# Kernel optimization log

Measured on AMD Instinct MI355X. Metric: run time of the kernel, lower is better.

Reference implementation:

```python
import jax, jax.numpy as jnp
import numpy as np

B, K, N, D, H, NNEG, NTOP = 8, 8, 128, 256, 128, 64, 64
UNARY_SCALES = (1.0, 1.0, 1.0)  # one scale per tree level, tree_height = log2(K) = 3


def setup_inputs():
    key = jax.random.key(0)
    ks = jax.random.split(key, 8)
    s = 0.05
    return {
        'pos_fea': jax.random.normal(ks[0], (B, K, N, D), jnp.float32),
        'neg_fea': jax.random.normal(ks[1], (B * K, NNEG, D), jnp.float32),
        'pos_classes': jax.random.randint(ks[2], (B, K, N), 0, 20),
        'target_class': jax.random.randint(ks[3], (B,), 0, 20),
        'Wp1': jax.random.normal(ks[4], (2 * D, H), jnp.float32) * s,
        'bp1': jnp.zeros((H,), jnp.float32),
        'Wp2': jax.random.normal(ks[5], (H, 1), jnp.float32) * s,
        'bp2': jnp.zeros((1,), jnp.float32),
        'Wu1': jax.random.normal(ks[6], (2 * D, H), jnp.float32) * s,
        'bu1': jnp.zeros((H,), jnp.float32),
        'Wu2': jax.random.normal(ks[7], (H, 1), jnp.float32) * s,
        'bu2': jnp.zeros((1,), jnp.float32),
    }


def _relation(f0, f1, W1, b1, W2, b2):
    # RelationModule: Dense(H, relu) -> Dense(1) applied to concat([f0_m, f1_n])
    # for every cross pair; concat-Dense is split into two GEMMs. -> [Bn, M0, M1]
    d = f0.shape[-1]
    h0 = jnp.einsum('bmd,dh->bmh', f0, W1[:d])
    h1 = jnp.einsum('bnd,dh->bnh', f1, W1[d:])
    h = jax.nn.relu(h0[:, :, None, :] + h1[:, None, :, :] + b1)
    return jnp.einsum('bmnh,h->bmn', h, W2[:, 0]) + b2[0]


def _bg(t, idx):
    # batched_gather along axis 1: t [Bn, P, ...], idx [Bn, T]
    ie = idx.reshape(idx.shape + (1,) * (t.ndim - 2))
    ie = jnp.broadcast_to(ie, idx.shape + t.shape[2:])
    return jnp.take_along_axis(t, ie, axis=1)


def _rep(fea, sub):
    # subproblem representative feature: fea [Bn,S,N,D], sub [Bn,M,S] -> [Bn,M,D]
    idx = jnp.swapaxes(sub, 1, 2)[..., None]              # [Bn,S,M,1]
    idx = jnp.broadcast_to(idx, idx.shape[:-1] + (fea.shape[-1],))
    return jnp.take_along_axis(fea, idx, axis=2).mean(axis=1)


def _tree(pos_fea, neg_fea, Wp1, bp1, Wp2, bp2, Wu1, bu1, Wu2, bu2):
    pos_flat = pos_fea.reshape(B * K, N, D)
    # UnaryModule: mean relation score of each positive proposal vs the negative bag
    ue = _relation(pos_flat, neg_fea, Wu1, bu1, Wu2, bu2).mean(-1)   # [B*K, N]
    sub = jnp.broadcast_to(jnp.arange(N, dtype=jnp.int32)[None, :, None], (B * K, N, 1))
    pe = jnp.zeros_like(ue)
    tree_height = int(np.log2(K))
    best = None
    for i in range(tree_height):
        S = 2 ** i                      # subproblem size per branch at this level
        Bn = sub.shape[0] // 2
        M = sub.shape[1]
        sub2 = sub.reshape(Bn, 2, M, S)  # [::2] / [1::2] split of adjacent rows
        sub0, sub1 = sub2[:, 0], sub2[:, 1]
        pe2 = pe.reshape(Bn, 2, M)
        ue2 = ue.reshape(Bn, 2, M)
        fea = pos_flat.reshape(Bn, 2, S, N, D)
        rep0 = _rep(fea[:, 0], sub0)
        rep1 = _rep(fea[:, 1], sub1)
        # PairwiseCrossSimilarity: scores for all cross pairs of candidates
        scores = _relation(rep0, rep1, Wp1, bp1, Wp2, bp2).reshape(Bn, M * M)
        p0 = jnp.repeat(jnp.arange(M), M)
        p1 = jnp.tile(jnp.arange(M), M)
        pe = pe2[:, 0][:, p0] + pe2[:, 1][:, p1] - scores
        ue = ue2[:, 0][:, p0] + ue2[:, 1][:, p1]
        total = pe + UNARY_SCALES[i] * ue
        sub = jnp.concatenate([sub0[:, p0], sub1[:, p1]], axis=-1)  # [Bn, M*M, 2S]
        topk = 1 if i == tree_height - 1 else min(M * M, NTOP)
        _, inds = jax.lax.top_k(-total, topk)
        sub = _bg(sub, inds)
        ue = jnp.take_along_axis(ue, inds, axis=1)
        pe = jnp.take_along_axis(pe, inds, axis=1)
        best = jnp.take_along_axis(total, inds, axis=1)
    return sub, best


def reference(pos_fea, neg_fea, pos_classes, target_class,
              Wp1, bp1, Wp2, bp2, Wu1, bu1, Wu2, bu2):
    sub, _ = _tree(pos_fea, neg_fea, Wp1, bp1, Wp2, bp2, Wu1, bu1, Wu2, bu2)
    is_target = (pos_classes == target_class[:, None, None]).astype(jnp.float32)
    return sub[:, 0], is_target  # selected proposal per image [B,K], [B,K,N]
```

## Files before the change

### kernel.cpp

```cpp
#include <hip/hip_runtime.h>
#include <stdint.h>

#define B_ 8
#define K_ 8
#define N_ 128
#define D_ 256
#define H_ 128
#define NNEG_ 64

typedef unsigned long long u64;

__device__ __forceinline__ u64 shfl_xor_u64(u64 v, int m) {
    int lo = __shfl_xor((int)(unsigned)v, m, 64);
    int hi = __shfl_xor((int)(unsigned)(v >> 32), m, 64);
    return ((u64)(unsigned)hi << 32) | (unsigned)lo;
}
__device__ __forceinline__ u64 bitonic_merge64(u64 m, int lane) {
#pragma unroll
    for (int j = 32; j > 0; j >>= 1) {
        u64 o = shfl_xor_u64(m, j);
        bool keepMin = ((lane & j) == 0);
        bool lt = m < o;
        m = (keepMin == lt) ? m : o;
    }
    return m;
}
__device__ __forceinline__ unsigned sortable(float f) {
    unsigned u = __float_as_uint(f);
    return (u & 0x80000000u) ? ~u : (u | 0x80000000u);
}
__device__ __forceinline__ float unsortable(unsigned u) {
    return __uint_as_float((u & 0x80000000u) ? (u & 0x7FFFFFFFu) : ~u);
}
__device__ __forceinline__ void sort128_wave0(u64* cand, int cc, int lane) {
    u64 v0 = (lane < cc) ? cand[lane] : ~0ull;
    u64 v1 = (64 + lane < cc) ? cand[64 + lane] : ~0ull;
#pragma unroll
    for (int k = 2; k <= 64; k <<= 1) {
        bool d0 = ((lane & k) == 0);
        bool d1 = (k == 64) ? false : d0;
#pragma unroll
        for (int j = k >> 1; j > 0; j >>= 1) {
            u64 o0 = shfl_xor_u64(v0, j);
            bool km0 = (((lane & j) == 0) == d0);
            v0 = (km0 == (v0 < o0)) ? v0 : o0;
            u64 o1 = shfl_xor_u64(v1, j);
            bool km1 = (((lane & j) == 0) == d1);
            v1 = (km1 == (v1 < o1)) ? v1 : o1;
        }
    }
    if (v0 > v1) { u64 tmp = v0; v0 = v1; v1 = tmp; }
#pragma unroll
    for (int j = 32; j > 0; j >>= 1) {
        bool km = ((lane & j) == 0);
        u64 o0 = shfl_xor_u64(v0, j);
        v0 = (km == (v0 < o0)) ? v0 : o0;
        u64 o1 = shfl_xor_u64(v1, j);
        v1 = (km == (v1 < o1)) ? v1 : o1;
    }
    cand[lane] = v0; cand[64 + lane] = v1;
}

__global__ __launch_bounds__(256) void g1_gemm(
    const float* __restrict__ pos, const float* __restrict__ neg,
    const float* __restrict__ Wu1, const float* __restrict__ Wp1,
    const int* __restrict__ pos_classes, const int* __restrict__ target_class,
    float* __restrict__ HU0, float* __restrict__ HU1n,
    float* __restrict__ HP0, float* __restrict__ HP1,
    float* __restrict__ outp) {
    int bid = blockIdx.x;
    int t = threadIdx.x;
    if (bid >= 448) {
        int base = (bid - 448) * 2048 + t * 8;
#pragma unroll
        for (int q = 0; q < 8; ++q) {
            int idx = base + q;
            outp[64 + idx] = (pos_classes[idx] == target_class[idx >> 10]) ? 1.0f : 0.0f;
        }
        return;
    }
    const float* A; const float* W; float* OUT; int rb;
    if (bid < 128)      { A = pos; W = Wu1;           OUT = HU0;  rb = bid * 64; }
    else if (bid < 192) { A = neg; W = Wu1 + D_ * H_; OUT = HU1n; rb = (bid - 128) * 64; }
    else if (bid < 320) { A = pos; W = Wp1;           OUT = HP0;  rb = (bid - 192) * 64; }
    else                { A = pos; W = Wp1 + D_ * H_; OUT = HP1;  rb = (bid - 320) * 64; }

    __shared__ float As[64][17];
    __shared__ float Bs[16][128];
    int tx = t & 15, ty = t >> 4;
    float acc[4][8];
#pragma unroll
    for (int i = 0; i < 4; ++i)
#pragma unroll
        for (int j = 0; j < 8; ++j) acc[i][j] = 0.f;

    for (int k0 = 0; k0 < D_; k0 += 16) {
        {
            int row = t >> 2, kq = (t & 3) * 4;
            const float4 av = *(const float4*)&A[(size_t)(rb + row) * D_ + k0 + kq];
            As[row][kq + 0] = av.x; As[row][kq + 1] = av.y;
            As[row][kq + 2] = av.z; As[row][kq + 3] = av.w;
        }
        {
            int flat = t * 8;
            int kr = flat >> 7, hc = flat & 127;
            float4 b0 = *(const float4*)&W[(size_t)(k0 + kr) * H_ + hc];
            float4 b1 = *(const float4*)&W[(size_t)(k0 + kr) * H_ + hc + 4];
            *(float4*)&Bs[kr][hc] = b0;
            *(float4*)&Bs[kr][hc + 4] = b1;
        }
        __syncthreads();
#pragma unroll
        for (int kk = 0; kk < 16; ++kk) {
            float a0 = As[ty * 4 + 0][kk], a1 = As[ty * 4 + 1][kk];
            float a2 = As[ty * 4 + 2][kk], a3 = As[ty * 4 + 3][kk];
            float bv[8];
            *(float4*)&bv[0] = *(const float4*)&Bs[kk][tx * 8];
            *(float4*)&bv[4] = *(const float4*)&Bs[kk][tx * 8 + 4];
#pragma unroll
            for (int j = 0; j < 8; ++j) {
                acc[0][j] += a0 * bv[j];
                acc[1][j] += a1 * bv[j];
                acc[2][j] += a2 * bv[j];
                acc[3][j] += a3 * bv[j];
            }
        }
        __syncthreads();
    }
#pragma unroll
    for (int i = 0; i < 4; ++i) {
        float4 o0 = {acc[i][0], acc[i][1], acc[i][2], acc[i][3]};
        float4 o1 = {acc[i][4], acc[i][5], acc[i][6], acc[i][7]};
        *(float4*)&OUT[(size_t)(rb + ty * 4 + i) * H_ + tx * 8] = o0;
        *(float4*)&OUT[(size_t)(rb + ty * 4 + i) * H_ + tx * 8 + 4] = o1;
    }
}

__global__ __launch_bounds__(256) void g2_ue_sc0(
    const float* __restrict__ HU0, const float* __restrict__ HU1n,
    const float* __restrict__ bu1, const float* __restrict__ Wu2,
    const float* __restrict__ bu2v,
    const float* __restrict__ HP0, const float* __restrict__ HP1,
    const float* __restrict__ bp1, const float* __restrict__ Wp2,
    const float* __restrict__ bp2,
    float* __restrict__ t0, float* __restrict__ sc0) {
    __shared__ float smem[13568];
    float (*Ls)[129] = (float(*)[129])smem;
    float (*Rs)[129] = (float(*)[129])(smem + 4128);
    float* wsv = smem + 4128 + 8256;
    float (*red)[33] = (float(*)[33])(smem + 4128 + 8256 + 128);

    int bid = blockIdx.x;
    int t = threadIdx.x;
    bool is_ue = bid < 256;

    if (is_ue) {
        int bk = bid >> 2, mt = bid & 3;
        for (int i = t; i < 64 * 128; i += 256) {
            int n = i >> 7, h = i & 127;
            Rs[n][h] = HU1n[(size_t)(bk * NNEG_ + n) * H_ + h];
        }
        for (int i = t; i < 32 * 128; i += 256) {
            int m = i >> 7, h = i & 127;
            Ls[m][h] = HU0[(size_t)(bk * N_ + mt * 32 + m) * H_ + h] + bu1[h];
        }
        if (t < 128) wsv[t] = Wu2[t];
    } else {
        int bid2 = bid - 256;
        int b = bid2 >> 3, m0t = (bid2 >> 1) & 3, m1t = bid2 & 1;
        const float* Lg = HP0 + (size_t)b * 2 * N_ * H_ + m0t * 32 * H_;
        const float* Rg = HP1 + (size_t)b * 2 * N_ * H_ + N_ * H_ + m1t * 64 * H_;
        for (int i = t; i < 64 * 128; i += 256) {
            int n = i >> 7, h = i & 127;
            Rs[n][h] = Rg[(size_t)n * H_ + h];
        }
        for (int i = t; i < 32 * 128; i += 256) {
            int m = i >> 7, h = i & 127;
            Ls[m][h] = Lg[(size_t)m * H_ + h] + bp1[h];
        }
        if (t < 128) wsv[t] = Wp2[t];
    }
    __syncthreads();

    int tm = t & 7, tn = t >> 3;
    const float* l0 = &Ls[tm * 4 + 0][0];
    const float* l1 = &Ls[tm * 4 + 1][0];
    const float* l2 = &Ls[tm * 4 + 2][0];
    const float* l3 = &Ls[tm * 4 + 3][0];
    const float* r0 = &Rs[tn * 2 + 0][0];
    const float* r1 = &Rs[tn * 2 + 1][0];
    float a00 = 0.f, a01 = 0.f, a10 = 0.f, a11 = 0.f;
    float a20 = 0.f, a21 = 0.f, a30 = 0.f, a31 = 0.f;
#pragma unroll 4
    for (int h = 0; h < 128; ++h) {
        float w = wsv[h];
        float b0 = r0[h], b1 = r1[h];
        float a0 = l0[h], a1 = l1[h], a2 = l2[h], a3 = l3[h];
        float v;
        v = a0 + b0; v = v > 0.f ? v : 0.f; a00 += v * w;
        v = a0 + b1; v = v > 0.f ? v : 0.f; a01 += v * w;
        v = a1 + b0; v = v > 0.f ? v : 0.f; a10 += v * w;
        v = a1 + b1; v = v > 0.f ? v : 0.f; a11 += v * w;
        v = a2 + b0; v = v > 0.f ? v : 0.f; a20 += v * w;
        v = a2 + b1; v = v > 0.f ? v : 0.f; a21 += v * w;
        v = a3 + b0; v = v > 0.f ? v : 0.f; a30 += v * w;
        v = a3 + b1; v = v > 0.f ? v : 0.f; a31 += v * w;
    }

    if (is_ue) {
        int bk = bid >> 2, mt = bid & 3;
        red[tm * 4 + 0][tn] = a00 + a01;
        red[tm * 4 + 1][tn] = a10 + a11;
        red[tm * 4 + 2][tn] = a20 + a21;
        red[tm * 4 + 3][tn] = a30 + a31;
        __syncthreads();
        if (t < 32) {
            float s = 0.f;
            for (int q = 0; q < 32; ++q) s += red[t][q];
            t0[bk * N_ + mt * 32 + t] = s * (1.0f / NNEG_) + bu2v[0];
        }
    } else {
        int bid2 = bid - 256;
        int b = bid2 >> 3, m0t = (bid2 >> 1) & 3, m1t = bid2 & 1;
        float bp2v = bp2[0];
        float* orow = sc0 + (size_t)b * 16384;
        float accs[4][2] = {{a00, a01}, {a10, a11}, {a20, a21}, {a30, a31}};
#pragma unroll
        for (int i = 0; i < 4; ++i) {
            int m0 = m0t * 32 + tm * 4 + i;
#pragma unroll
            for (int j = 0; j < 2; ++j) {
                int m1 = m1t * 64 + tn * 2 + j;
                orow[m0 * 128 + m1] = accs[i][j] + bp2v;
            }
        }
    }
}

__global__ __launch_bounds__(1024) void g3_top0(const float* __restrict__ sc0,
                                                const float* __restrict__ t0,
                                                float* __restrict__ tA,
                                                int* __restrict__ pA) {
    int r = blockIdx.x;
    int t = threadIdx.x, lane = t & 63;
    __shared__ float tt[256];
    __shared__ unsigned cnt[16][2];
    __shared__ unsigned ccnt;
    __shared__ u64 cand[128];
    if (t < 256) tt[t] = t0[r * 256 + t];
    if (t < 32) cnt[t >> 1][t & 1] = 0u;
    if (t == 0) ccnt = 0u;
    __syncthreads();
    const float* row = sc0 + (size_t)r * 16384;
    unsigned sv[16];
#pragma unroll
    for (int j = 0; j < 16; ++j) {
        int idx = j * 1024 + t;
        float v = (tt[idx >> 7] + tt[128 + (idx & 127)]) - row[idx];
        sv[j] = sortable(v);
    }
    unsigned T = 0u;
#pragma unroll
    for (int it = 0; it < 16; ++it) {
        int p = 30 - 2 * it;
        unsigned C1 = T | (1u << p), C2 = T | (2u << p), C3 = T | (3u << p);
        unsigned c13 = 0u, c2 = 0u;
#pragma unroll
        for (int j = 0; j < 16; ++j) {
            c13 += (sv[j] < C1) ? 1u : 0u;
            c13 += (sv[j] < C3) ? 0x10000u : 0u;
            c2 += (sv[j] < C2) ? 1u : 0u;
        }
#pragma unroll
        for (int off = 32; off > 0; off >>= 1) {
            c13 += (unsigned)__shfl_xor((int)c13, off, 64);
            c2 += (unsigned)__shfl_xor((int)c2, off, 64);
        }
        if (lane == 0) { atomicAdd(&cnt[it][0], c13); atomicAdd(&cnt[it][1], c2); }
        __syncthreads();
        unsigned t13 = cnt[it][0], t2v = cnt[it][1];
        unsigned t1 = t13 & 0xFFFFu, t3 = t13 >> 16;
        unsigned k = (t3 < 64u) ? 3u : (t2v < 64u) ? 2u : (t1 < 64u) ? 1u : 0u;
        T |= (k << p);
    }
#pragma unroll
    for (int j = 0; j < 16; ++j) {
        if (sv[j] <= T) {
            unsigned pos = atomicAdd(&ccnt, 1u);
            if (pos < 128u) {
                int idx = j * 1024 + t;
                cand[pos] = ((u64)sv[j] << 32) | (unsigned)idx;
            }
        }
    }
    __syncthreads();
    if (t < 64) {
        int cc = (int)(ccnt < 128u ? ccnt : 128u);
        sort128_wave0(cand, cc, lane);
        u64 kk = cand[lane];
        int idx = (int)(kk & 0xFFFFFFFFull);
        tA[r * 64 + lane] = unsortable((unsigned)(kk >> 32));
        pA[r * 64 + lane] = ((idx >> 7) << 8) | (idx & 127);
    }
}

__global__ __launch_bounds__(256) void g4a_s1(
    const float* __restrict__ HP0, const float* __restrict__ HP1,
    const float* __restrict__ tA, const int* __restrict__ pA,
    const float* __restrict__ bp1, const float* __restrict__ Wp2,
    const float* __restrict__ bp2, u64* __restrict__ g4top) {
    int bid = blockIdx.x;
    int u = bid >> 1, half = bid & 1;
    int t = threadIdx.x, lane = t & 63, w = t >> 6;
    __shared__ float LsT[128][68];
    __shared__ float RsT[128][36];
    __shared__ float taL[64], taR[64];
    __shared__ int paL[64], paR[64];
    __shared__ float wsv[128];
    __shared__ unsigned cnt[16][2];
    __shared__ unsigned ccnt;
    __shared__ u64 cand[128];
    if (t < 64) { taL[t] = tA[(2 * u) * 64 + t]; paL[t] = pA[(2 * u) * 64 + t]; }
    else if (t < 128) { int e = t - 64; taR[e] = tA[(2 * u + 1) * 64 + e]; paR[e] = pA[(2 * u + 1) * 64 + e]; }
    if (t < 128) wsv[t] = Wp2[t];
    if (t < 32) cnt[t >> 1][t & 1] = 0u;
    if (t == 0) ccnt = 0u;
    float bp2v = bp2[0];
    __syncthreads();
    for (int i = t; i < 64 * 128; i += 256) {
        int m = i >> 7, h = i & 127;
        int pk = paL[m]; int a0 = pk >> 8, a1 = pk & 255;
        float s = HP0[(size_t)(4 * u) * 16384 + a0 * 128 + h]
                + HP0[(size_t)(4 * u + 1) * 16384 + a1 * 128 + h];
        LsT[h][m] = s * 0.5f + bp1[h];
    }
    for (int i = t; i < 32 * 128; i += 256) {
        int n = i >> 7, h = i & 127;
        int ng = half * 32 + n;
        int pk = paR[ng]; int c0 = pk >> 8, c1 = pk & 255;
        float s = HP1[(size_t)(4 * u + 2) * 16384 + c0 * 128 + h]
                + HP1[(size_t)(4 * u + 3) * 16384 + c1 * 128 + h];
        RsT[h][n] = s * 0.5f;
    }
    __syncthreads();
    int qm = w * 4 + (lane >> 4);
    int qn = lane & 15;
    float acc[4][2];
#pragma unroll
    for (int i = 0; i < 4; ++i) { acc[i][0] = 0.f; acc[i][1] = 0.f; }
#pragma unroll 2
    for (int h = 0; h < 128; ++h) {
        float4 lv = *(const float4*)&LsT[h][qm * 4];
        float2 rv = *(const float2*)&RsT[h][qn * 2];
        float wv = wsv[h];
        float v;
        v = lv.x + rv.x; v = v > 0.f ? v : 0.f; acc[0][0] += v * wv;
        v = lv.x + rv.y; v = v > 0.f ? v : 0.f; acc[0][1] += v * wv;
        v = lv.y + rv.x; v = v > 0.f ? v : 0.f; acc[1][0] += v * wv;
        v = lv.y + rv.y; v = v > 0.f ? v : 0.f; acc[1][1] += v * wv;
        v = lv.z + rv.x; v = v > 0.f ? v : 0.f; acc[2][0] += v * wv;
        v = lv.z + rv.y; v = v > 0.f ? v : 0.f; acc[2][1] += v * wv;
        v = lv.w + rv.x; v = v > 0.f ? v : 0.f; acc[3][0] += v * wv;
        v = lv.w + rv.y; v = v > 0.f ? v : 0.f; acc[3][1] += v * wv;
    }
    unsigned sv[8];
#pragma unroll
    for (int mi = 0; mi < 4; ++mi) {
#pragma unroll
        for (int nj = 0; nj < 2; ++nj) {
            int m = qm * 4 + mi;
            int ng = half * 32 + qn * 2 + nj;
            float val = (taL[m] + taR[ng]) - (acc[mi][nj] + bp2v);
            sv[mi * 2 + nj] = sortable(val);
        }
    }
    unsigned T = 0u;
#pragma unroll
    for (int it = 0; it < 16; ++it) {
        int p = 30 - 2 * it;
        unsigned C1 = T | (1u << p), C2 = T | (2u << p), C3 = T | (3u << p);
        unsigned c13 = 0u, c2 = 0u;
#pragma unroll
        for (int j = 0; j < 8; ++j) {
            c13 += (sv[j] < C1) ? 1u : 0u;
            c13 += (sv[j] < C3) ? 0x10000u : 0u;
            c2 += (sv[j] < C2) ? 1u : 0u;
        }
#pragma unroll
        for (int off = 32; off > 0; off >>= 1) {
            c13 += (unsigned)__shfl_xor((int)c13, off, 64);
            c2 += (unsigned)__shfl_xor((int)c2, off, 64);
        }
        if (lane == 0) { atomicAdd(&cnt[it][0], c13); atomicAdd(&cnt[it][1], c2); }
        __syncthreads();
        unsigned t13 = cnt[it][0], t2v = cnt[it][1];
        unsigned t1 = t13 & 0xFFFFu, t3 = t13 >> 16;
        unsigned k = (t3 < 64u) ? 3u : (t2v < 64u) ? 2u : (t1 < 64u) ? 1u : 0u;
        T |= (k << p);
    }
#pragma unroll
    for (int j = 0; j < 8; ++j) {
        if (sv[j] <= T) {
            unsigned pos = atomicAdd(&ccnt, 1u);
            if (pos < 128u) {
                int mi = j >> 1, nj = j & 1;
                int idx = (qm * 4 + mi) * 64 + half * 32 + qn * 2 + nj;
                cand[pos] = ((u64)sv[j] << 32) | (unsigned)idx;
            }
        }
    }
    __syncthreads();
    if (w == 0) {
        int cc = (int)(ccnt < 128u ? ccnt : 128u);
        sort128_wave0(cand, cc, lane);
        g4top[(size_t)bid * 64 + lane] = cand[lane];
    }
}

__global__ __launch_bounds__(256) void g4b_s2(
    const float* __restrict__ HP0, const float* __restrict__ HP1,
    const int* __restrict__ pA, const u64* __restrict__ g4top,
    const float* __restrict__ bp1, const float* __restrict__ Wp2,
    const float* __restrict__ bp2, float* __restrict__ outp) {
    int b = blockIdx.x;
    int t = threadIdx.x, lane = t & 63, w = t >> 6;
    __shared__ float LsT[128][68];
    __shared__ float RsT[128][36];
    __shared__ float tL[64], tR[64];
    __shared__ unsigned subL[64], subR[64];
    __shared__ float wsv[128];
    __shared__ u64 sred[4];
    if (t < 128) wsv[t] = Wp2[t];
    float bp2v = bp2[0];
    if (w < 2) {
        const u64* A = g4top + (size_t)(4 * b + 2 * w) * 64;
        const u64* Bp = g4top + (size_t)(4 * b + 2 * w + 1) * 64;
        u64 x = A[lane], y = Bp[63 - lane];
        u64 m = x < y ? x : y;
        m = bitonic_merge64(m, lane);
        int idx = (int)(m & 0xFFFFFFFFull);
        int p0 = idx >> 6, p1 = idx & 63;
        float val = unsortable((unsigned)(m >> 32));
        int rowL = 4 * b + 2 * w;
        int pkL = pA[rowL * 64 + p0];
        int pkR = pA[(rowL + 1) * 64 + p1];
        unsigned leaves = ((unsigned)pkL << 16) | (unsigned)pkR;
        if (w == 0) { tL[lane] = val; subL[lane] = leaves; }
        else        { tR[lane] = val; subR[lane] = leaves; }
    }
    __syncthreads();
    for (int i = t; i < 64 * 128; i += 256) {
        int m = i >> 7, h = i & 127;
        unsigned s4 = subL[m];
        float s = HP0[(size_t)(8 * b + 0) * 16384 + ((s4 >> 24) & 255u) * 128 + h]
                + HP0[(size_t)(8 * b + 1) * 16384 + ((s4 >> 16) & 255u) * 128 + h]
                + HP0[(size_t)(8 * b + 2) * 16384 + ((s4 >> 8) & 255u) * 128 + h]
                + HP0[(size_t)(8 * b + 3) * 16384 + (s4 & 255u) * 128 + h];
        LsT[h][m] = s * 0.25f + bp1[h];
    }
    u64 best = ~0ull;
    int qm = w * 4 + (lane >> 4);
    int qn = lane & 15;
    for (int half = 0; half < 2; ++half) {
        __syncthreads();
        for (int i = t; i < 32 * 128; i += 256) {
            int n = i >> 7, h = i & 127;
            int ng = half * 32 + n;
            unsigned s4 = subR[ng];
            float s = HP1[(size_t)(8 * b + 4) * 16384 + ((s4 >> 24) & 255u) * 128 + h]
                    + HP1[(size_t)(8 * b + 5) * 16384 + ((s4 >> 16) & 255u) * 128 + h]
                    + HP1[(size_t)(8 * b + 6) * 16384 + ((s4 >> 8) & 255u) * 128 + h]
                    + HP1[(size_t)(8 * b + 7) * 16384 + (s4 & 255u) * 128 + h];
            RsT[h][n] = s * 0.25f;
        }
        __syncthreads();
        float acc[4][2];
#pragma unroll
        for (int i = 0; i < 4; ++i) { acc[i][0] = 0.f; acc[i][1] = 0.f; }
#pragma unroll 2
        for (int h = 0; h < 128; ++h) {
            float4 lv = *(const float4*)&LsT[h][qm * 4];
            float2 rv = *(const float2*)&RsT[h][qn * 2];
            float wv = wsv[h];
            float v;
            v = lv.x + rv.x; v = v > 0.f ? v : 0.f; acc[0][0] += v * wv;
            v = lv.x + rv.y; v = v > 0.f ? v : 0.f; acc[0][1] += v * wv;
            v = lv.y + rv.x; v = v > 0.f ? v : 0.f; acc[1][0] += v * wv;
            v = lv.y + rv.y; v = v > 0.f ? v : 0.f; acc[1][1] += v * wv;
            v = lv.z + rv.x; v = v > 0.f ? v : 0.f; acc[2][0] += v * wv;
            v = lv.z + rv.y; v = v > 0.f ? v : 0.f; acc[2][1] += v * wv;
            v = lv.w + rv.x; v = v > 0.f ? v : 0.f; acc[3][0] += v * wv;
            v = lv.w + rv.y; v = v > 0.f ? v : 0.f; acc[3][1] += v * wv;
        }
#pragma unroll
        for (int mi = 0; mi < 4; ++mi) {
#pragma unroll
            for (int nj = 0; nj < 2; ++nj) {
                int m = qm * 4 + mi;
                int ng = half * 32 + qn * 2 + nj;
                float val = (tL[m] + tR[ng]) - (acc[mi][nj] + bp2v);
                u64 kk = ((u64)sortable(val) << 32) | (unsigned)(m * 64 + ng);
                best = kk < best ? kk : best;
            }
        }
    }
#pragma unroll
    for (int off = 32; off > 0; off >>= 1) {
        u64 o = shfl_xor_u64(best, off);
        best = o < best ? o : best;
    }
    if (lane == 0) sred[w] = best;
    __syncthreads();
    if (t == 0) {
        u64 bb = sred[0];
        for (int p = 1; p < 4; ++p) { u64 o = sred[p]; bb = o < bb ? o : bb; }
        int idx = (int)(bb & 0xFFFFFFFFull);
        unsigned sl = subL[idx >> 6], sr = subR[idx & 63];
        outp[b * 8 + 0] = (float)((sl >> 24) & 255u);
        outp[b * 8 + 1] = (float)((sl >> 16) & 255u);
        outp[b * 8 + 2] = (float)((sl >> 8) & 255u);
        outp[b * 8 + 3] = (float)(sl & 255u);
        outp[b * 8 + 4] = (float)((sr >> 24) & 255u);
        outp[b * 8 + 5] = (float)((sr >> 16) & 255u);
        outp[b * 8 + 6] = (float)((sr >> 8) & 255u);
        outp[b * 8 + 7] = (float)(sr & 255u);
    }
}

extern "C" void kernel_launch(void* const* d_in, const int* in_sizes, int n_in,
                              void* d_out, int out_size, void* d_ws, size_t ws_size,
                              hipStream_t stream) {
    const float* pos = (const float*)d_in[0];
    const float* neg = (const float*)d_in[1];
    const int* pos_classes = (const int*)d_in[2];
    const int* target_class = (const int*)d_in[3];
    const float* Wp1 = (const float*)d_in[4];
    const float* bp1 = (const float*)d_in[5];
    const float* Wp2 = (const float*)d_in[6];
    const float* bp2 = (const float*)d_in[7];
    const float* Wu1 = (const float*)d_in[8];
    const float* bu1 = (const float*)d_in[9];
    const float* Wu2 = (const float*)d_in[10];
    const float* bu2 = (const float*)d_in[11];

    float* wsf = (float*)d_ws;
    float* HU0 = wsf;
    float* HP0 = HU0 + 1048576;
    float* HP1 = HP0 + 1048576;
    float* HU1n = HP1 + 1048576;
    float* t0 = HU1n + 524288;
    float* sc0 = t0 + 8192;
    float* tA = sc0 + 524288;
    int* pA = (int*)(tA + 2048);
    u64* g4top = (u64*)(pA + 2048);
    float* outp = (float*)d_out;

    g1_gemm<<<452, 256, 0, stream>>>(pos, neg, Wu1, Wp1, pos_classes,
                                     target_class, HU0, HU1n, HP0, HP1, outp);
    g2_ue_sc0<<<512, 256, 0, stream>>>(HU0, HU1n, bu1, Wu2, bu2,
                                       HP0, HP1, bp1, Wp2, bp2, t0, sc0);
    g3_top0<<<32, 1024, 0, stream>>>(sc0, t0, tA, pA);
    g4a_s1<<<32, 256, 0, stream>>>(HP0, HP1, tA, pA, bp1, Wp2, bp2, g4top);
    g4b_s2<<<8, 256, 0, stream>>>(HP0, HP1, pA, g4top, bp1, Wp2, bp2, outp);
}
```

Before: 209.2 us.

## Split top-k selection across more blocks with per-wave select and merge trees

The level-0 top-64 selection now runs per wave on 512-element chunks across 256 blocks. Each wave does a ballot-based radix select with no block barriers, then bitonic-sorts its candidates, and a separate small kernel merges the 8 partial lists per row. The level-1 pair scoring is spread over 128 blocks with smaller tiles, and its radix select is replaced by a direct 128-element register sort per wave plus merges. The intent is to lift the low block counts and the barrier- and atomic-heavy selection loops. In exchange it adds one more launch and an extra global round trip for the partial lists, and it reuses the start of the workspace (HU0) for the candidate buffers.

```diff
diff --git a/kernel.cpp b/kernel.cpp
--- a/kernel.cpp
+++ b/kernel.cpp
@@ -25,6 +25,11 @@
     }
     return m;
 }
+__device__ __forceinline__ u64 merge2(u64 a, u64 b, int lane) {
+    u64 br = shfl_xor_u64(b, 63);
+    u64 m = a < br ? a : br;
+    return bitonic_merge64(m, lane);
+}
 __device__ __forceinline__ unsigned sortable(float f) {
     unsigned u = __float_as_uint(f);
     return (u & 0x80000000u) ? ~u : (u | 0x80000000u);
@@ -32,9 +37,7 @@
 __device__ __forceinline__ float unsortable(unsigned u) {
     return __uint_as_float((u & 0x80000000u) ? (u & 0x7FFFFFFFu) : ~u);
 }
-__device__ __forceinline__ void sort128_wave0(u64* cand, int cc, int lane) {
-    u64 v0 = (lane < cc) ? cand[lane] : ~0ull;
-    u64 v1 = (64 + lane < cc) ? cand[64 + lane] : ~0ull;
+__device__ __forceinline__ void sort128_reg(u64& v0, u64& v1, int lane) {
 #pragma unroll
     for (int k = 2; k <= 64; k <<= 1) {
         bool d0 = ((lane & k) == 0);
@@ -58,7 +61,6 @@
         u64 o1 = shfl_xor_u64(v1, j);
         v1 = (km == (v1 < o1)) ? v1 : o1;
     }
-    cand[lane] = v0; cand[64 + lane] = v1;
 }
 
 __global__ __launch_bounds__(256) void g1_gemm(
@@ -237,71 +239,83 @@
     }
 }
 
-__global__ __launch_bounds__(1024) void g3_top0(const float* __restrict__ sc0,
+__global__ __launch_bounds__(256) void g3a_top0(const float* __restrict__ sc0,
                                                 const float* __restrict__ t0,
+                                                u64* __restrict__ g3c) {
+    int bid = blockIdx.x;
+    int r = bid >> 3, c = bid & 7;
+    int t = threadIdx.x, lane = t & 63, w = t >> 6;
+    __shared__ float tt[256];
+    __shared__ u64 cand[4][128];
+    if (t < 256) tt[t] = t0[r * 256 + t];
+    __syncthreads();
+    const float* row = sc0 + (size_t)r * 16384 + c * 2048 + w * 512;
+    unsigned sv[8];
+#pragma unroll
+    for (int j = 0; j < 8; ++j) {
+        int li = j * 64 + lane;
+        int idx = c * 2048 + w * 512 + li;
+        float v = (tt[idx >> 7] + tt[128 + (idx & 127)]) - row[li];
+        sv[j] = sortable(v);
+    }
+    unsigned T = 0u;
+#pragma unroll
+    for (int it = 0; it < 16; ++it) {
+        int p = 30 - 2 * it;
+        unsigned C1 = T | (1u << p), C2 = T | (2u << p), C3 = T | (3u << p);
+        unsigned c1 = 0u, c2 = 0u, c3 = 0u;
+#pragma unroll
+        for (int j = 0; j < 8; ++j) {
+            c1 += (unsigned)__popcll(__ballot(sv[j] < C1));
+            c2 += (unsigned)__popcll(__ballot(sv[j] < C2));
+            c3 += (unsigned)__popcll(__ballot(sv[j] < C3));
+        }
+        unsigned k = (c3 < 64u) ? 3u : (c2 < 64u) ? 2u : (c1 < 64u) ? 1u : 0u;
+        T |= (k << p);
+    }
+    u64* my = cand[w];
+    int base = 0;
+#pragma unroll
+    for (int j = 0; j < 8; ++j) {
+        u64 mask = __ballot(sv[j] <= T);
+        if (sv[j] <= T) {
+            int pos = base + (int)__popcll(mask & ((1ull << lane) - 1ull));
+            if (pos < 128) {
+                int idx = c * 2048 + w * 512 + j * 64 + lane;
+                my[pos] = ((u64)sv[j] << 32) | (unsigned)idx;
+            }
+        }
+        base += (int)__popcll(mask);
+    }
+    int cc = base < 128 ? base : 128;
+    u64 v0 = (lane < cc) ? my[lane] : ~0ull;
+    u64 v1 = (64 + lane < cc) ? my[64 + lane] : ~0ull;
+    sort128_reg(v0, v1, lane);
+    my[lane] = v0;
+    __syncthreads();
+    if (w == 0) {
+        u64 x0 = cand[0][lane], x1 = cand[1][lane];
+        u64 x2 = cand[2][lane], x3 = cand[3][lane];
+        u64 y0 = merge2(x0, x1, lane), y1 = merge2(x2, x3, lane);
+        g3c[(size_t)bid * 64 + lane] = merge2(y0, y1, lane);
+    }
+}
+
+__global__ __launch_bounds__(64) void g3b_merge(const u64* __restrict__ g3c,
                                                 float* __restrict__ tA,
                                                 int* __restrict__ pA) {
     int r = blockIdx.x;
-    int t = threadIdx.x, lane = t & 63;
-    __shared__ float tt[256];
-    __shared__ unsigned cnt[16][2];
-    __shared__ unsigned ccnt;
-    __shared__ u64 cand[128];
-    if (t < 256) tt[t] = t0[r * 256 + t];
-    if (t < 32) cnt[t >> 1][t & 1] = 0u;
-    if (t == 0) ccnt = 0u;
-    __syncthreads();
-    const float* row = sc0 + (size_t)r * 16384;
-    unsigned sv[16];
-#pragma unroll
-    for (int j = 0; j < 16; ++j) {
-        int idx = j * 1024 + t;
-        float v = (tt[idx >> 7] + tt[128 + (idx & 127)]) - row[idx];
-        sv[j] = sortable(v);
-    }
-    unsigned T = 0u;
-#pragma unroll
-    for (int it = 0; it < 16; ++it) {
-        int p = 30 - 2 * it;
-        unsigned C1 = T | (1u << p), C2 = T | (2u << p), C3 = T | (3u << p);
-        unsigned c13 = 0u, c2 = 0u;
-#pragma unroll
-        for (int j = 0; j < 16; ++j) {
-            c13 += (sv[j] < C1) ? 1u : 0u;
-            c13 += (sv[j] < C3) ? 0x10000u : 0u;
-            c2 += (sv[j] < C2) ? 1u : 0u;
-        }
-#pragma unroll
-        for (int off = 32; off > 0; off >>= 1) {
-            c13 += (unsigned)__shfl_xor((int)c13, off, 64);
-            c2 += (unsigned)__shfl_xor((int)c2, off, 64);
-        }
-        if (lane == 0) { atomicAdd(&cnt[it][0], c13); atomicAdd(&cnt[it][1], c2); }
-        __syncthreads();
-        unsigned t13 = cnt[it][0], t2v = cnt[it][1];
-        unsigned t1 = t13 & 0xFFFFu, t3 = t13 >> 16;
-        unsigned k = (t3 < 64u) ? 3u : (t2v < 64u) ? 2u : (t1 < 64u) ? 1u : 0u;
-        T |= (k << p);
-    }
-#pragma unroll
-    for (int j = 0; j < 16; ++j) {
-        if (sv[j] <= T) {
-            unsigned pos = atomicAdd(&ccnt, 1u);
-            if (pos < 128u) {
-                int idx = j * 1024 + t;
-                cand[pos] = ((u64)sv[j] << 32) | (unsigned)idx;
-            }
-        }
-    }
-    __syncthreads();
-    if (t < 64) {
-        int cc = (int)(ccnt < 128u ? ccnt : 128u);
-        sort128_wave0(cand, cc, lane);
-        u64 kk = cand[lane];
-        int idx = (int)(kk & 0xFFFFFFFFull);
-        tA[r * 64 + lane] = unsortable((unsigned)(kk >> 32));
-        pA[r * 64 + lane] = ((idx >> 7) << 8) | (idx & 127);
-    }
+    int lane = threadIdx.x;
+    const u64* Lp = g3c + (size_t)r * 512;
+    u64 x0 = Lp[lane], x1 = Lp[64 + lane], x2 = Lp[128 + lane], x3 = Lp[192 + lane];
+    u64 x4 = Lp[256 + lane], x5 = Lp[320 + lane], x6 = Lp[384 + lane], x7 = Lp[448 + lane];
+    u64 y0 = merge2(x0, x1, lane), y1 = merge2(x2, x3, lane);
+    u64 y2 = merge2(x4, x5, lane), y3 = merge2(x6, x7, lane);
+    u64 z0 = merge2(y0, y1, lane), z1 = merge2(y2, y3, lane);
+    u64 f = merge2(z0, z1, lane);
+    int idx = (int)(f & 0xFFFFFFFFull);
+    tA[r * 64 + lane] = unsortable((unsigned)(f >> 32));
+    pA[r * 64 + lane] = ((idx >> 7) << 8) | (idx & 127);
 }
 
 __global__ __launch_bounds__(256) void g4a_s1(
@@ -310,24 +324,20 @@
     const float* __restrict__ bp1, const float* __restrict__ Wp2,
     const float* __restrict__ bp2, u64* __restrict__ g4top) {
     int bid = blockIdx.x;
-    int u = bid >> 1, half = bid & 1;
+    int u = bid >> 3, mq = (bid >> 1) & 3, nh = bid & 1;
     int t = threadIdx.x, lane = t & 63, w = t >> 6;
-    __shared__ float LsT[128][68];
-    __shared__ float RsT[128][36];
-    __shared__ float taL[64], taR[64];
-    __shared__ int paL[64], paR[64];
+    __shared__ float LsT[128][17];
+    __shared__ float RsT[128][34];
+    __shared__ float taL[16], taR[32];
+    __shared__ int paL[16], paR[32];
     __shared__ float wsv[128];
-    __shared__ unsigned cnt[16][2];
-    __shared__ unsigned ccnt;
-    __shared__ u64 cand[128];
-    if (t < 64) { taL[t] = tA[(2 * u) * 64 + t]; paL[t] = pA[(2 * u) * 64 + t]; }
-    else if (t < 128) { int e = t - 64; taR[e] = tA[(2 * u + 1) * 64 + e]; paR[e] = pA[(2 * u + 1) * 64 + e]; }
-    if (t < 128) wsv[t] = Wp2[t];
-    if (t < 32) cnt[t >> 1][t & 1] = 0u;
-    if (t == 0) ccnt = 0u;
+    __shared__ u64 cand[4][64];
+    if (t < 16) { taL[t] = tA[(2 * u) * 64 + mq * 16 + t]; paL[t] = pA[(2 * u) * 64 + mq * 16 + t]; }
+    else if (t < 48) { int e = t - 16; taR[e] = tA[(2 * u + 1) * 64 + nh * 32 + e]; paR[e] = pA[(2 * u + 1) * 64 + nh * 32 + e]; }
+    if (t >= 128) wsv[t - 128] = Wp2[t - 128];
     float bp2v = bp2[0];
     __syncthreads();
-    for (int i = t; i < 64 * 128; i += 256) {
+    for (int i = t; i < 16 * 128; i += 256) {
         int m = i >> 7, h = i & 127;
         int pk = paL[m]; int a0 = pk >> 8, a1 = pk & 255;
         float s = HP0[(size_t)(4 * u) * 16384 + a0 * 128 + h]
@@ -336,84 +346,38 @@
     }
     for (int i = t; i < 32 * 128; i += 256) {
         int n = i >> 7, h = i & 127;
-        int ng = half * 32 + n;
-        int pk = paR[ng]; int c0 = pk >> 8, c1 = pk & 255;
+        int pk = paR[n]; int c0 = pk >> 8, c1 = pk & 255;
         float s = HP1[(size_t)(4 * u + 2) * 16384 + c0 * 128 + h]
                 + HP1[(size_t)(4 * u + 3) * 16384 + c1 * 128 + h];
         RsT[h][n] = s * 0.5f;
     }
     __syncthreads();
-    int qm = w * 4 + (lane >> 4);
-    int qn = lane & 15;
-    float acc[4][2];
-#pragma unroll
-    for (int i = 0; i < 4; ++i) { acc[i][0] = 0.f; acc[i][1] = 0.f; }
-#pragma unroll 2
+    int lm = w * 4 + (lane >> 4);
+    int ln = lane & 15;
+    float a0 = 0.f, a1 = 0.f;
+#pragma unroll 4
     for (int h = 0; h < 128; ++h) {
-        float4 lv = *(const float4*)&LsT[h][qm * 4];
-        float2 rv = *(const float2*)&RsT[h][qn * 2];
+        float lv = LsT[h][lm];
+        float2 rv = *(const float2*)&RsT[h][ln * 2];
         float wv = wsv[h];
         float v;
-        v = lv.x + rv.x; v = v > 0.f ? v : 0.f; acc[0][0] += v * wv;
-        v = lv.x + rv.y; v = v > 0.f ? v : 0.f; acc[0][1] += v * wv;
-        v = lv.y + rv.x; v = v > 0.f ? v : 0.f; acc[1][0] += v * wv;
-        v = lv.y + rv.y; v = v > 0.f ? v : 0.f; acc[1][1] += v * wv;
-        v = lv.z + rv.x; v = v > 0.f ? v : 0.f; acc[2][0] += v * wv;
-        v = lv.z + rv.y; v = v > 0.f ? v : 0.f; acc[2][1] += v * wv;
-        v = lv.w + rv.x; v = v > 0.f ? v : 0.f; acc[3][0] += v * wv;
-        v = lv.w + rv.y; v = v > 0.f ? v : 0.f; acc[3][1] += v * wv;
-    }
-    unsigned sv[8];
-#pragma unroll
-    for (int mi = 0; mi < 4; ++mi) {
-#pragma unroll
-        for (int nj = 0; nj < 2; ++nj) {
-            int m = qm * 4 + mi;
-            int ng = half * 32 + qn * 2 + nj;
-            float val = (taL[m] + taR[ng]) - (acc[mi][nj] + bp2v);
-            sv[mi * 2 + nj] = sortable(val);
-        }
-    }
-    unsigned T = 0u;
-#pragma unroll
-    for (int it = 0; it < 16; ++it) {
-        int p = 30 - 2 * it;
-        unsigned C1 = T | (1u << p), C2 = T | (2u << p), C3 = T | (3u << p);
-        unsigned c13 = 0u, c2 = 0u;
-#pragma unroll
-        for (int j = 0; j < 8; ++j) {
-            c13 += (sv[j] < C1) ? 1u : 0u;
-            c13 += (sv[j] < C3) ? 0x10000u : 0u;
-            c2 += (sv[j] < C2) ? 1u : 0u;
-        }
-#pragma unroll
-        for (int off = 32; off > 0; off >>= 1) {
-            c13 += (unsigned)__shfl_xor((int)c13, off, 64);
-            c2 += (unsigned)__shfl_xor((int)c2, off, 64);
-        }
-        if (lane == 0) { atomicAdd(&cnt[it][0], c13); atomicAdd(&cnt[it][1], c2); }
-        __syncthreads();
-        unsigned t13 = cnt[it][0], t2v = cnt[it][1];
-        unsigned t1 = t13 & 0xFFFFu, t3 = t13 >> 16;
-        unsigned k = (t3 < 64u) ? 3u : (t2v < 64u) ? 2u : (t1 < 64u) ? 1u : 0u;
-        T |= (k << p);
-    }
-#pragma unroll
-    for (int j = 0; j < 8; ++j) {
-        if (sv[j] <= T) {
-            unsigned pos = atomicAdd(&ccnt, 1u);
-            if (pos < 128u) {
-                int mi = j >> 1, nj = j & 1;
-                int idx = (qm * 4 + mi) * 64 + half * 32 + qn * 2 + nj;
-                cand[pos] = ((u64)sv[j] << 32) | (unsigned)idx;
-            }
-        }
-    }
+        v = lv + rv.x; v = v > 0.f ? v : 0.f; a0 += v * wv;
+        v = lv + rv.y; v = v > 0.f ? v : 0.f; a1 += v * wv;
+    }
+    int m_unit = mq * 16 + lm;
+    int n0 = nh * 32 + ln * 2;
+    float val0 = (taL[lm] + taR[ln * 2 + 0]) - (a0 + bp2v);
+    float val1 = (taL[lm] + taR[ln * 2 + 1]) - (a1 + bp2v);
+    u64 v0 = ((u64)sortable(val0) << 32) | (unsigned)(m_unit * 64 + n0);
+    u64 v1 = ((u64)sortable(val1) << 32) | (unsigned)(m_unit * 64 + n0 + 1);
+    sort128_reg(v0, v1, lane);
+    cand[w][lane] = v0;
     __syncthreads();
     if (w == 0) {
-        int cc = (int)(ccnt < 128u ? ccnt : 128u);
-        sort128_wave0(cand, cc, lane);
-        g4top[(size_t)bid * 64 + lane] = cand[lane];
+        u64 x0 = cand[0][lane], x1 = cand[1][lane];
+        u64 x2 = cand[2][lane], x3 = cand[3][lane];
+        u64 y0 = merge2(x0, x1, lane), y1 = merge2(x2, x3, lane);
+        g4top[(size_t)bid * 64 + lane] = merge2(y0, y1, lane);
     }
 }
 
@@ -433,11 +397,13 @@
     if (t < 128) wsv[t] = Wp2[t];
     float bp2v = bp2[0];
     if (w < 2) {
-        const u64* A = g4top + (size_t)(4 * b + 2 * w) * 64;
-        const u64* Bp = g4top + (size_t)(4 * b + 2 * w + 1) * 64;
-        u64 x = A[lane], y = Bp[63 - lane];
-        u64 m = x < y ? x : y;
-        m = bitonic_merge64(m, lane);
+        const u64* Lp = g4top + (size_t)(2 * b + w) * 512;
+        u64 x0 = Lp[lane], x1 = Lp[64 + lane], x2 = Lp[128 + lane], x3 = Lp[192 + lane];
+        u64 x4 = Lp[256 + lane], x5 = Lp[320 + lane], x6 = Lp[384 + lane], x7 = Lp[448 + lane];
+        u64 y0 = merge2(x0, x1, lane), y1 = merge2(x2, x3, lane);
+        u64 y2 = merge2(x4, x5, lane), y3 = merge2(x6, x7, lane);
+        u64 z0 = merge2(y0, y1, lane), z1 = merge2(y2, y3, lane);
+        u64 m = merge2(z0, z1, lane);
         int idx = (int)(m & 0xFFFFFFFFull);
         int p0 = idx >> 6, p1 = idx & 63;
         float val = unsortable((unsigned)(m >> 32));
@@ -552,14 +518,16 @@
     float* sc0 = t0 + 8192;
     float* tA = sc0 + 524288;
     int* pA = (int*)(tA + 2048);
-    u64* g4top = (u64*)(pA + 2048);
+    u64* g3c = (u64*)wsf;
+    u64* g4top = (u64*)wsf + 16384;
     float* outp = (float*)d_out;
 
     g1_gemm<<<452, 256, 0, stream>>>(pos, neg, Wu1, Wp1, pos_classes,
                                      target_class, HU0, HU1n, HP0, HP1, outp);
     g2_ue_sc0<<<512, 256, 0, stream>>>(HU0, HU1n, bu1, Wu2, bu2,
                                        HP0, HP1, bp1, Wp2, bp2, t0, sc0);
-    g3_top0<<<32, 1024, 0, stream>>>(sc0, t0, tA, pA);
-    g4a_s1<<<32, 256, 0, stream>>>(HP0, HP1, tA, pA, bp1, Wp2, bp2, g4top);
+    g3a_top0<<<256, 256, 0, stream>>>(sc0, t0, g3c);
+    g3b_merge<<<32, 64, 0, stream>>>(g3c, tA, pA);
+    g4a_s1<<<128, 256, 0, stream>>>(HP0, HP1, tA, pA, bp1, Wp2, bp2, g4top);
     g4b_s2<<<8, 256, 0, stream>>>(HP0, HP1, pA, g4top, bp1, Wp2, bp2, outp);
 }
```

Result: faster. 180.3 us (-13.8%).
